# Kernel optimization log

Hardware: AMD Instinct MI355X
Metric: run time of the kernel (lower is better)

The kernel has to match this reference:

```python
import jax, jax.numpy as jnp
import numpy as np

TOKENS, HIDDEN, N_EXPERTS = 16384, 2048, 64
JITTER_EPS = 0.01
Z_LOSS_COEFF = 0.001


def setup_inputs() -> dict:
    key = jax.random.key(0)
    k1, k2 = jax.random.split(key)
    x = jax.random.normal(k1, (TOKENS, HIDDEN), dtype=jnp.float32)
    w = jax.random.normal(k2, (N_EXPERTS, HIDDEN), dtype=jnp.float32) * 0.02  # router weight [E,H]
    return {"x": x, "w": w}


def _route_pass(scores_sel, scores, jitter_eps):
    # scores_sel: logits possibly with -inf at already-selected expert (top-2 pass)
    # scores:     original logits (used for abs/clamp factor, as in torch code)
    mx = jnp.max(scores_sel, axis=-1, keepdims=True)                      # [N,1]
    factor = jnp.maximum(jnp.abs(scores), mx)                             # scores.abs().clamp(min=mx)
    mask = jax.lax.stop_gradient((mx - scores) / factor > 2.0 * jitter_eps)
    masked_logits = jnp.where(mask, -jnp.inf, scores_sel)
    # eval path (training=False): selected_experts = argmax of (masked-for-selection) scores
    sel = jnp.argmax(scores_sel, axis=-1)[..., None]                      # [N,1] int
    gates = jax.nn.softmax(masked_logits, axis=-1)
    # mask_for_one: selected == argmax(gates) holds deterministically in eval -> 1.0
    mult = jnp.take_along_axis(gates, sel, axis=-1)                       # [N,1]
    return mult, sel


def reference(x, w):
    logits = x @ w.T                                                      # [N,E]
    # z-loss (identity on logits in forward; scalar returned for completeness)
    z_loss = Z_LOSS_COEFF * jnp.mean(jnp.square(jax.nn.logsumexp(logits, axis=-1)))
    original_gates = jax.nn.softmax(logits, axis=-1)
    # top-1 pass
    m1, s1 = _route_pass(logits, logits, JITTER_EPS)
    # top-2 pass: mask out the first selection
    e_idx = jnp.arange(logits.shape[-1])[None, :]
    scores2 = jnp.where(e_idx == s1, -jnp.inf, logits)
    m2, s2 = _route_pass(scores2, logits, JITTER_EPS)
    multiplier = jnp.concatenate([m1, m2], axis=-1)                       # [N,2]
    selected_experts = jnp.concatenate([s1, s2], axis=-1)                 # [N,2]
    return multiplier, original_gates, selected_experts, z_loss
```

## Files before the change

kernel.cpp:

```cpp
#include <hip/hip_runtime.h>
#include <math.h>

#define TOKENS 16384
#define HIDDEN 2048
#define NEXP   64
#define MT     16
#define NBLK   (TOKENS / MT)

#define GATES_OFF (TOKENS * 2)
#define SEL_OFF   (GATES_OFF + TOKENS * NEXP)
#define Z_OFF     (SEL_OFF + TOKENS * 2)

#define WIMG_BYTES (NEXP * HIDDEN * 2 * 2)

typedef __attribute__((ext_vector_type(8))) _Float16 f16x8;
typedef __attribute__((ext_vector_type(4))) float    f32x4;

__device__ __forceinline__ float wave_sum64(float v) {
    #pragma unroll
    for (int s = 1; s < 64; s <<= 1) v += __shfl_xor(v, s, 64);
    return v;
}

__global__ __launch_bounds__(256) void wconvert(
    const float* __restrict__ w, uint4* __restrict__ wimg)
{
    const int s = blockIdx.x * 256 + threadIdx.x;
    const int c    = s >> 10;
    const int r    = s & 1023;
    const int l    = r & 63;
    const int nt   = (r >> 6) & 1;
    const int kh   = (r >> 7) & 1;
    const int term = (r >> 8) & 1;
    const int eh   = (r >> 9) & 1;
    const int e = eh * 32 + nt * 16 + (l & 15);
    const int k = c * 64 + kh * 32 + (l >> 4) * 8;

    const float* src = w + (size_t)e * HIDDEN + k;
    union { _Float16 f[8]; uint4 u; } o;
    #pragma unroll
    for (int j = 0; j < 8; ++j) {
        const float v = src[j];
        const _Float16 h = (_Float16)v;
        o.f[j] = (term == 0) ? h : (_Float16)((v - (float)h) * 4096.f);
    }
    wimg[s] = o.u;
}

__device__ __forceinline__ void cvt_split(const float4 a, const float4 b,
                                          f16x8& hi, f16x8& lo) {
    union { _Float16 f[8]; f16x8 v; } H, L;
    #pragma unroll
    for (int j = 0; j < 4; ++j) {
        const float s0 = (&a.x)[j];
        const float s1 = (&b.x)[j];
        const _Float16 h0 = (_Float16)s0;
        const _Float16 h1 = (_Float16)s1;
        H.f[j]     = h0;
        H.f[j + 4] = h1;
        L.f[j]     = (_Float16)((s0 - (float)h0) * 4096.f);
        L.f[j + 4] = (_Float16)((s1 - (float)h1) * 4096.f);
    }
    hi = H.v; lo = L.v;
}

struct Stage {
    float4 a0, a1;
    f16x8  bh[4], bl[4];
};

__device__ __forceinline__ void load_stage(Stage& S, const float* ax0,
                                           const uint4* wB, int s) {
    S.a0 = *(const float4*)(ax0 + s * 32);
    S.a1 = *(const float4*)(ax0 + s * 32 + 4);
    const uint4* p = wB + (s >> 1) * 1024 + (s & 1) * 128;
    S.bh[0] = *(const f16x8*)(p);
    S.bh[1] = *(const f16x8*)(p + 64);
    S.bh[2] = *(const f16x8*)(p + 512);
    S.bh[3] = *(const f16x8*)(p + 576);
    S.bl[0] = *(const f16x8*)(p + 256);
    S.bl[1] = *(const f16x8*)(p + 320);
    S.bl[2] = *(const f16x8*)(p + 768);
    S.bl[3] = *(const f16x8*)(p + 832);
}

__device__ __forceinline__ void consume_stage(
    const Stage& S, f32x4 (&acc0)[4], f32x4 (&acc1)[4])
{
    f16x8 Ah, Al;
    cvt_split(S.a0, S.a1, Ah, Al);
    #pragma unroll
    for (int g = 0; g < 4; ++g) {
        acc0[g] = __builtin_amdgcn_mfma_f32_16x16x32_f16(Ah, S.bh[g], acc0[g], 0, 0, 0);
        acc1[g] = __builtin_amdgcn_mfma_f32_16x16x32_f16(Ah, S.bl[g], acc1[g], 0, 0, 0);
        acc1[g] = __builtin_amdgcn_mfma_f32_16x16x32_f16(Al, S.bh[g], acc1[g], 0, 0, 0);
    }
}

__global__ __launch_bounds__(256, 3) void router_main(
    const float* __restrict__ x, const uint4* __restrict__ wimg,
    float* __restrict__ out, float* __restrict__ zpartial)
{
    __shared__ __align__(16) float lg[4][MT * 66];
    __shared__ float zred[4];

    const int tid  = threadIdx.x;
    const int wv   = __builtin_amdgcn_readfirstlane(tid >> 6);
    const int lane = tid & 63;
    const int t0   = blockIdx.x * MT;

    const float* ax0 = x + (size_t)(t0 + (lane & 15)) * HIDDEN
                         + wv * 512 + (lane >> 4) * 8;

    const uint4* wB = wimg + wv * 8192 + lane;

    f32x4 acc0[4], acc1[4];
    #pragma unroll
    for (int g = 0; g < 4; ++g) { acc0[g] = (f32x4)0.f; acc1[g] = (f32x4)0.f; }

    Stage SA, SB;
    load_stage(SA, ax0, wB, 0);
    load_stage(SB, ax0, wB, 1);
    __builtin_amdgcn_sched_barrier(0);

    #pragma unroll
    for (int s = 0; s < 16; s += 2) {
        consume_stage(SA, acc0, acc1);
        if (s + 2 < 16) load_stage(SA, ax0, wB, s + 2);
        __builtin_amdgcn_sched_barrier(0);

        consume_stage(SB, acc0, acc1);
        if (s + 3 < 16) load_stage(SB, ax0, wB, s + 3);
        __builtin_amdgcn_sched_barrier(0);
    }

    #pragma unroll
    for (int g = 0; g < 4; ++g)
        #pragma unroll
        for (int r = 0; r < 4; ++r) {
            const int tok = (lane >> 4) * 4 + r;
            const int e   = (g >> 1) * 32 + (g & 1) * 16 + (lane & 15);
            lg[wv][tok * 66 + e] = acc0[g][r] + acc1[g][r] * (1.f / 4096.f);
        }
    __syncthreads();

    float zsum = 0.f;
    for (int tt = 0; tt < 4; ++tt) {
        const int t = wv * 4 + tt;
        const int li = t * 66 + lane;
        const float v = lg[0][li] + lg[1][li] + lg[2][li] + lg[3][li];

        float bv = v; int bi = lane;
        #pragma unroll
        for (int s = 1; s < 64; s <<= 1) {
            const float ov = __shfl_xor(bv, s, 64);
            const int   oi = __shfl_xor(bi, s, 64);
            if (ov > bv || (ov == bv && oi < bi)) { bv = ov; bi = oi; }
        }
        const float max1 = bv; const int s1 = bi;

        const float e1 = expf(v - max1);
        const float sume = wave_sum64(e1);
        out[GATES_OFF + (size_t)(t0 + t) * NEXP + lane] = e1 / sume;
        const float lse = max1 + logf(sume);
        zsum += lse * lse;

        const bool mask1 = (max1 - v) > 0.02f * fmaxf(fabsf(v), max1);
        const float sum1 = wave_sum64(mask1 ? 0.f : e1);

        float bv2 = (lane == s1) ? -INFINITY : v; int bi2 = lane;
        #pragma unroll
        for (int s = 1; s < 64; s <<= 1) {
            const float ov = __shfl_xor(bv2, s, 64);
            const int   oi = __shfl_xor(bi2, s, 64);
            if (ov > bv2 || (ov == bv2 && oi < bi2)) { bv2 = ov; bi2 = oi; }
        }
        const float max2 = bv2; const int s2 = bi2;

        const bool mask2 = (max2 - v) > 0.02f * fmaxf(fabsf(v), max2);
        const float p2v = (mask2 || lane == s1) ? 0.f : expf(v - max2);
        const float sum2 = wave_sum64(p2v);

        if (lane == 0) {
            const size_t trow = (size_t)(t0 + t) * 2;
            out[trow + 0] = 1.f / sum1;
            out[trow + 1] = 1.f / sum2;
            out[SEL_OFF + trow + 0] = (float)s1;
            out[SEL_OFF + trow + 1] = (float)s2;
        }
    }

    if (lane == 0) zred[wv] = zsum;
    __syncthreads();
    if (tid == 0)
        zpartial[blockIdx.x] = zred[0] + zred[1] + zred[2] + zred[3];
}

__global__ __launch_bounds__(256) void zfinal(
    const float* __restrict__ zpartial, float* __restrict__ out)
{
    const int tid = threadIdx.x;
    float v = zpartial[tid] + zpartial[tid + 256]
            + zpartial[tid + 512] + zpartial[tid + 768];
    v = wave_sum64(v);
    __shared__ float red[4];
    if ((tid & 63) == 0) red[tid >> 6] = v;
    __syncthreads();
    if (tid == 0) {
        const float tot = red[0] + red[1] + red[2] + red[3];
        out[Z_OFF] = 0.001f * (tot / (float)TOKENS);
    }
}

extern "C" void kernel_launch(void* const* d_in, const int* in_sizes, int n_in,
                              void* d_out, int out_size, void* d_ws, size_t ws_size,
                              hipStream_t stream) {
    const float* x = (const float*)d_in[0];
    const float* w = (const float*)d_in[1];
    float* out = (float*)d_out;

    uint4* wimg     = (uint4*)d_ws;
    float* zpartial = (float*)((char*)d_ws + WIMG_BYTES);

    wconvert<<<128, 256, 0, stream>>>(w, wimg);
    router_main<<<NBLK, 256, 0, stream>>>(x, wimg, out, zpartial);
    zfinal<<<1, 256, 0, stream>>>(zpartial, out);
}
```

Before: 218.8 us.

## Stage x tiles through LDS with async global_load_lds double buffering

```diff
diff --git a/kernel.cpp b/kernel.cpp
--- a/kernel.cpp
+++ b/kernel.cpp
@@ -6,6 +6,9 @@
 #define NEXP   64
 #define MT     16
 #define NBLK   (TOKENS / MT)
+#define BK     256
+#define NCH    (HIDDEN / BK)
+#define ROWB   1024
 
 #define GATES_OFF (TOKENS * 2)
 #define SEL_OFF   (GATES_OFF + TOKENS * NEXP)
@@ -20,6 +23,12 @@
     #pragma unroll
     for (int s = 1; s < 64; s <<= 1) v += __shfl_xor(v, s, 64);
     return v;
+}
+
+__device__ __forceinline__ void dma16(const void* g, void* l) {
+    __builtin_amdgcn_global_load_lds(
+        (const __attribute__((address_space(1))) unsigned int*)g,
+        (__attribute__((address_space(3))) unsigned int*)l, 16, 0, 0);
 }
 
 __global__ __launch_bounds__(256) void wconvert(
@@ -64,83 +73,92 @@
     hi = H.v; lo = L.v;
 }
 
-struct Stage {
-    float4 a0, a1;
-    f16x8  bh[4], bl[4];
-};
-
-__device__ __forceinline__ void load_stage(Stage& S, const float* ax0,
-                                           const uint4* wB, int s) {
-    S.a0 = *(const float4*)(ax0 + s * 32);
-    S.a1 = *(const float4*)(ax0 + s * 32 + 4);
-    const uint4* p = wB + (s >> 1) * 1024 + (s & 1) * 128;
-    S.bh[0] = *(const f16x8*)(p);
-    S.bh[1] = *(const f16x8*)(p + 64);
-    S.bh[2] = *(const f16x8*)(p + 512);
-    S.bh[3] = *(const f16x8*)(p + 576);
-    S.bl[0] = *(const f16x8*)(p + 256);
-    S.bl[1] = *(const f16x8*)(p + 320);
-    S.bl[2] = *(const f16x8*)(p + 768);
-    S.bl[3] = *(const f16x8*)(p + 832);
-}
-
-__device__ __forceinline__ void consume_stage(
-    const Stage& S, f32x4 (&acc0)[4], f32x4 (&acc1)[4])
-{
-    f16x8 Ah, Al;
-    cvt_split(S.a0, S.a1, Ah, Al);
-    #pragma unroll
-    for (int g = 0; g < 4; ++g) {
-        acc0[g] = __builtin_amdgcn_mfma_f32_16x16x32_f16(Ah, S.bh[g], acc0[g], 0, 0, 0);
-        acc1[g] = __builtin_amdgcn_mfma_f32_16x16x32_f16(Ah, S.bl[g], acc1[g], 0, 0, 0);
-        acc1[g] = __builtin_amdgcn_mfma_f32_16x16x32_f16(Al, S.bh[g], acc1[g], 0, 0, 0);
-    }
-}
-
 __global__ __launch_bounds__(256, 3) void router_main(
     const float* __restrict__ x, const uint4* __restrict__ wimg,
     float* __restrict__ out, float* __restrict__ zpartial)
 {
-    __shared__ __align__(16) float lg[4][MT * 66];
+    __shared__ __align__(16) unsigned char smem[2 * MT * ROWB];
     __shared__ float zred[4];
+    float* lg = (float*)smem;
 
     const int tid  = threadIdx.x;
     const int wv   = __builtin_amdgcn_readfirstlane(tid >> 6);
     const int lane = tid & 63;
     const int t0   = blockIdx.x * MT;
 
-    const float* ax0 = x + (size_t)(t0 + (lane & 15)) * HIDDEN
-                         + wv * 512 + (lane >> 4) * 8;
-
-    const uint4* wB = wimg + wv * 8192 + lane;
+    const int row_r = lane & 15;
+    const int kgrp  = lane >> 4;
+    const int sr    = (row_r & 7) << 4;
+
+    const float* xg[4];
+    #pragma unroll
+    for (int p = 0; p < 4; ++p) {
+        const int row  = wv * 4 + p;
+        const int srow = (row & 7) << 4;
+        xg[p] = x + (size_t)(t0 + row) * HIDDEN + (((lane * 16) ^ srow) >> 2);
+    }
 
     f32x4 acc0[4], acc1[4];
     #pragma unroll
     for (int g = 0; g < 4; ++g) { acc0[g] = (f32x4)0.f; acc1[g] = (f32x4)0.f; }
 
-    Stage SA, SB;
-    load_stage(SA, ax0, wB, 0);
-    load_stage(SB, ax0, wB, 1);
-    __builtin_amdgcn_sched_barrier(0);
-
-    #pragma unroll
-    for (int s = 0; s < 16; s += 2) {
-        consume_stage(SA, acc0, acc1);
-        if (s + 2 < 16) load_stage(SA, ax0, wB, s + 2);
-        __builtin_amdgcn_sched_barrier(0);
-
-        consume_stage(SB, acc0, acc1);
-        if (s + 3 < 16) load_stage(SB, ax0, wB, s + 3);
-        __builtin_amdgcn_sched_barrier(0);
+    #pragma unroll
+    for (int p = 0; p < 4; ++p)
+        dma16(xg[p], smem + (wv * 4 + p) * ROWB);
+    __syncthreads();
+
+    #pragma unroll
+    for (int c = 0; c < NCH; ++c) {
+        const int buf = c & 1;
+
+        const uint4* p0 = wimg + (size_t)(c * 4 + wv) * 1024 + lane;
+        f16x8 bh[2][4], bl[2][4];
+        #pragma unroll
+        for (int st = 0; st < 2; ++st) {
+            const uint4* p = p0 + st * 128;
+            bh[st][0] = *(const f16x8*)(p);
+            bh[st][1] = *(const f16x8*)(p + 64);
+            bh[st][2] = *(const f16x8*)(p + 512);
+            bh[st][3] = *(const f16x8*)(p + 576);
+            bl[st][0] = *(const f16x8*)(p + 256);
+            bl[st][1] = *(const f16x8*)(p + 320);
+            bl[st][2] = *(const f16x8*)(p + 768);
+            bl[st][3] = *(const f16x8*)(p + 832);
+        }
+
+        if (c + 1 < NCH) {
+            #pragma unroll
+            for (int p = 0; p < 4; ++p)
+                dma16(xg[p] + (c + 1) * BK,
+                      smem + (buf ^ 1) * (MT * ROWB) + (wv * 4 + p) * ROWB);
+        }
+
+        const unsigned char* abase = smem + buf * (MT * ROWB) + row_r * ROWB;
+        #pragma unroll
+        for (int st = 0; st < 2; ++st) {
+            const int kb0 = wv * 256 + st * 128 + kgrp * 32;
+            const float4 va = *(const float4*)(abase + (kb0 ^ sr));
+            const float4 vb = *(const float4*)(abase + ((kb0 + 16) ^ sr));
+            f16x8 Ah, Al;
+            cvt_split(va, vb, Ah, Al);
+            #pragma unroll
+            for (int g = 0; g < 4; ++g) {
+                acc0[g] = __builtin_amdgcn_mfma_f32_16x16x32_f16(Ah, bh[st][g], acc0[g], 0, 0, 0);
+                acc1[g] = __builtin_amdgcn_mfma_f32_16x16x32_f16(Ah, bl[st][g], acc1[g], 0, 0, 0);
+                acc1[g] = __builtin_amdgcn_mfma_f32_16x16x32_f16(Al, bh[st][g], acc1[g], 0, 0, 0);
+            }
+        }
+
+        __syncthreads();
     }
 
     #pragma unroll
     for (int g = 0; g < 4; ++g)
         #pragma unroll
         for (int r = 0; r < 4; ++r) {
-            const int tok = (lane >> 4) * 4 + r;
-            const int e   = (g >> 1) * 32 + (g & 1) * 16 + (lane & 15);
-            lg[wv][tok * 66 + e] = acc0[g][r] + acc1[g][r] * (1.f / 4096.f);
+            const int tok = kgrp * 4 + r;
+            const int e   = (g >> 1) * 32 + (g & 1) * 16 + row_r;
+            lg[wv * (MT * 66) + tok * 66 + e] = acc0[g][r] + acc1[g][r] * (1.f / 4096.f);
         }
     __syncthreads();
 
@@ -148,7 +166,8 @@
     for (int tt = 0; tt < 4; ++tt) {
         const int t = wv * 4 + tt;
         const int li = t * 66 + lane;
-        const float v = lg[0][li] + lg[1][li] + lg[2][li] + lg[3][li];
+        const float v = lg[0 * (MT * 66) + li] + lg[1 * (MT * 66) + li]
+                      + lg[2 * (MT * 66) + li] + lg[3 * (MT * 66) + li];
 
         float bv = v; int bi = lane;
         #pragma unroll
```

New measurement: 213.6 us. -2.4%, faster.
